# Performance work log

Measured on AMD Instinct MI355X. Metric: run time of the kernel, lower is better.

The kernel has to match this reference:

```python
import jax, jax.numpy as jnp
import numpy as np

B, S = 256, 512
NQ = 1000           # n_skills
MEM, DK, DV, FC = 20, 50, 200, 50  # memory_size, key dim, value dim, final fc dim


def _kaiming(key, shape, fan_in):
    return jax.random.normal(key, shape) * np.float32(np.sqrt(2.0 / fan_in))


def setup_inputs() -> dict:
    key = jax.random.key(0)
    ks = jax.random.split(key, 12)
    q_data = jax.random.randint(ks[0], (B, S), 0, NQ + 1)
    qa_data = jax.random.randint(ks[1], (B, S), 0, 2 * NQ + 1)
    u = jax.random.uniform(ks[2], (B * S,))
    # target: -1 = masked/padding, else binary label (matches target.ge(0) masking)
    target = jnp.where(u < 0.1, -1.0, (u > 0.55).astype(jnp.float32))
    q_embed_w = _kaiming(ks[3], (NQ + 1, DK), DK)
    qa_embed_w = _kaiming(ks[4], (2 * NQ + 1, DV), DV)
    memory_key = _kaiming(ks[5], (MEM, DK), DK)
    init_memory_value = _kaiming(ks[6], (MEM, DV), DV)
    erase_w = _kaiming(ks[7], (DV, DV), DV)
    erase_b = jnp.zeros((DV,), jnp.float32)
    add_w = _kaiming(ks[8], (DV, DV), DV)
    add_b = jnp.zeros((DV,), jnp.float32)
    read_w = _kaiming(ks[9], (DV + FC, FC), DV + FC)
    read_b = jnp.zeros((FC,), jnp.float32)
    pred_w = _kaiming(ks[10], (FC, 1), FC)
    pred_b = jnp.zeros((1,), jnp.float32)
    return dict(q_data=q_data, qa_data=qa_data, target=target,
                q_embed_w=q_embed_w, qa_embed_w=qa_embed_w,
                memory_key=memory_key, init_memory_value=init_memory_value,
                erase_w=erase_w, erase_b=erase_b, add_w=add_w, add_b=add_b,
                read_w=read_w, read_b=read_b, pred_w=pred_w, pred_b=pred_b)


def reference(q_data, qa_data, target, q_embed_w, qa_embed_w, memory_key,
              init_memory_value, erase_w, erase_b, add_w, add_b,
              read_w, read_b, pred_w, pred_b):
    b = q_data.shape[0]
    q_e = q_embed_w[q_data]     # [B,S,DK]
    qa_e = qa_embed_w[qa_data]  # [B,S,DV]
    Mv0 = jnp.broadcast_to(init_memory_value, (b, MEM, DV))

    def step(Mv, xs):
        q_t, qa_t = xs                                        # [B,DK], [B,DV]
        corr = jax.nn.softmax(q_t @ memory_key.T, axis=1)     # [B,MEM] addressing
        read = jnp.einsum('bm,bmd->bd', corr, Mv)             # weighted read
        erase = jax.nn.sigmoid(qa_t @ erase_w + erase_b)      # [B,DV]
        add = jnp.tanh(qa_t @ add_w + add_b)                  # [B,DV]
        w = corr[:, :, None]                                  # [B,MEM,1]
        Mv = Mv * (1.0 - w * erase[:, None, :]) + w * add[:, None, :]
        return Mv, read

    _, reads = jax.lax.scan(step, Mv0, (q_e.transpose(1, 0, 2), qa_e.transpose(1, 0, 2)))
    reads = reads.transpose(1, 0, 2)                          # [B,S,DV]
    x = jnp.concatenate([reads, q_e], axis=-1)                # [B,S,DV+FC]
    h = jnp.tanh(x @ read_w + read_b)                         # [B,S,FC]
    logits = (h @ pred_w + pred_b).reshape(-1)                # [B*S]
    mask = target >= 0.0
    t = jnp.where(mask, target, 0.0)
    # numerically-stable BCE-with-logits, masked mean
    bce = jnp.maximum(logits, 0.0) - logits * t + jnp.log1p(jnp.exp(-jnp.abs(logits)))
    loss = jnp.sum(jnp.where(mask, bce, 0.0)) / jnp.maximum(mask.sum(), 1)
    return loss, jax.nn.sigmoid(logits)
```

## Files before the change

### kernel.cpp

```cpp
#include <hip/hip_runtime.h>
#include <math.h>

#define B_   256
#define S_   512
#define NQ_  1000
#define MEM_ 20
#define DK_  50
#define DV_  200
#define FC_  50
#define RPB  2
#define CHK  16
#define CLEN (S_/CHK)
#define NKS  7
#define XS_STRIDE 232
#define CORR_STRIDE 12
#define NB_EA    ((2*NQ_+1+RPB-1)/RPB)
#define NB_CORR  4
#define NB_WPACK 7
#define NB_HQ    251
#define PREP1_BLOCKS (NB_EA+NB_CORR)
#define MM_BLOCKS (B_*CHK)
#define SCANA_BLOCKS (B_*(CHK-1))
#define SCANA_TOTAL (SCANA_BLOCKS+NB_WPACK+NB_HQ)

typedef __attribute__((ext_vector_type(8))) short bf16x8_t;
typedef __attribute__((ext_vector_type(4))) float f32x4_t;
typedef __attribute__((ext_vector_type(2))) _Float16 f16x2_t;

static __device__ __forceinline__ f16x2_t h2(unsigned u){ return __builtin_bit_cast(f16x2_t, u); }
static __device__ __forceinline__ unsigned h2u(f16x2_t v){ return __builtin_bit_cast(unsigned, v); }
static __device__ __forceinline__ unsigned packh2(float x, float y){
  unsigned short bx = __builtin_bit_cast(unsigned short, (_Float16)x);
  unsigned short by = __builtin_bit_cast(unsigned short, (_Float16)y);
  return (unsigned)bx | ((unsigned)by << 16);
}
static __device__ __forceinline__ f16x2_t pkfma16(f16x2_t a, f16x2_t b, f16x2_t c){
  return __builtin_elementwise_fma(a, b, c);
}
static __device__ __forceinline__ f16x2_t splat_l(f16x2_t p){ return __builtin_shufflevector(p, p, 0, 0); }
static __device__ __forceinline__ f16x2_t splat_h(f16x2_t p){ return __builtin_shufflevector(p, p, 1, 1); }

static __device__ __forceinline__ unsigned short f2bf(float f){
  unsigned u = __float_as_uint(f);
  unsigned r = u + 0x7fffu + ((u >> 16) & 1u);
  return (unsigned short)(r >> 16);
}
static __device__ __forceinline__ float ftanh(float x){
  float e = __expf(2.f*x);
  return 1.f - 2.f*__builtin_amdgcn_rcpf(e+1.f);
}
static __device__ __forceinline__ float fsigm(float x){
  return __builtin_amdgcn_rcpf(1.f+__expf(-x));
}

__global__ __launch_bounds__(256) void k_prep1(
    const float* __restrict__ qaw,
    const float* __restrict__ ew, const float* __restrict__ eb,
    const float* __restrict__ aw, const float* __restrict__ ab,
    unsigned* __restrict__ eaTab,
    const float* __restrict__ qw, const float* __restrict__ mk,
    unsigned* __restrict__ corrH){
  __shared__ float qa[RPB*DV_];
  int blk = blockIdx.x;
  if(blk < NB_EA){
    int row0 = blk*RPB;
    for(int i=threadIdx.x; i<RPB*DV_; i+=256){
      int r = i/DV_, cc = i - r*DV_;
      int row = row0 + r;
      qa[i] = (row <= 2*NQ_) ? qaw[row*DV_+cc] : 0.f;
    }
    __syncthreads();
    int d = threadIdx.x;
    if(d >= DV_) return;
    float accE[RPB], accA[RPB];
    #pragma unroll
    for(int r=0;r<RPB;++r){ accE[r] = eb[d]; accA[r] = ab[d]; }
    float we0 = ew[d], wa0 = aw[d];
    for(int j=0;j<DV_;++j){
      int jn = (j+1 < DV_) ? j+1 : j;
      float we1 = ew[jn*DV_+d];
      float wa1 = aw[jn*DV_+d];
      #pragma unroll
      for(int r=0;r<RPB;++r){
        float x = qa[r*DV_+j];
        accE[r] = fmaf(x, we0, accE[r]);
        accA[r] = fmaf(x, wa0, accA[r]);
      }
      we0 = we1; wa0 = wa1;
    }
    #pragma unroll
    for(int r=0;r<RPB;++r){
      int row = row0 + r;
      if(row <= 2*NQ_){
        unsigned he = (unsigned)__builtin_bit_cast(unsigned short, (_Float16)fsigm(accE[r]));
        unsigned ha = (unsigned)__builtin_bit_cast(unsigned short, (_Float16)ftanh(accA[r]));
        eaTab[(size_t)row*DV_+d] = he | (ha << 16);
      }
    }
  } else {
    int q = (blk-NB_EA)*256 + threadIdx.x;
    if(q > NQ_) return;
    float qv[DK_];
    #pragma unroll
    for(int j=0;j<DK_;++j) qv[j] = qw[q*DK_+j];
    float s[MEM_]; float mx = -1e30f;
    #pragma unroll
    for(int m=0;m<MEM_;++m){
      float acc = 0.f;
      #pragma unroll
      for(int j=0;j<DK_;++j) acc = fmaf(qv[j], mk[m*DK_+j], acc);
      s[m] = acc; mx = fmaxf(mx, acc);
    }
    float sum = 0.f;
    #pragma unroll
    for(int m=0;m<MEM_;++m){ s[m] = __expf(s[m]-mx); sum += s[m]; }
    float inv = __builtin_amdgcn_rcpf(sum);
    #pragma unroll
    for(int i=0;i<MEM_/2;++i)
      corrH[q*CORR_STRIDE+i] = packh2(s[2*i]*inv, s[2*i+1]*inv);
  }
}

__global__ __launch_bounds__(256,8) void k_scanA(const int* __restrict__ qd,
    const int* __restrict__ qad,
    const unsigned* __restrict__ corrH,
    const unsigned* __restrict__ eaTab,
    unsigned* __restrict__ ABu,
    const float* __restrict__ qw,
    const float* __restrict__ rw, const float* __restrict__ rb,
    const float* __restrict__ pw,
    unsigned short* __restrict__ WpFrag, float* __restrict__ pwPad,
    float* __restrict__ hq){
  const int blk = blockIdx.x;
  if(blk >= SCANA_BLOCKS){
    int xblk = blk - SCANA_BLOCKS;
    if(xblk < NB_WPACK){
      int ks = xblk;
      int nt = threadIdx.x >> 6;
      int lane = threadIdx.x & 63;
      int quad = lane >> 4, col = lane & 15;
      int n = nt*16 + col;
      unsigned short tmp[8];
      #pragma unroll
      for(int j=0;j<8;++j){
        int k = ks*32 + quad*8 + j;
        tmp[j] = (k < DV_ && n < FC_) ? f2bf(rw[k*FC_+n]) : (unsigned short)0;
      }
      uint4* dst = reinterpret_cast<uint4*>(WpFrag + ((size_t)(ks*4+nt)*64 + lane)*8);
      *dst = *reinterpret_cast<const uint4*>(tmp);
      if(ks == 0 && threadIdx.x < 64)
        pwPad[threadIdx.x] = (threadIdx.x < FC_) ? pw[threadIdx.x] : 0.f;
    } else {
      int idx = (xblk-NB_WPACK)*256 + threadIdx.x;
      int q = idx >> 6, n = idx & 63;
      if(q > NQ_) return;
      float v = 0.f;
      if(n < FC_){
        float acc = rb[n];
        #pragma unroll
        for(int j=0;j<DK_;++j)
          acc = fmaf(qw[q*DK_+j], rw[(DV_+j)*FC_+n], acc);
        v = acc;
      }
      hq[q*64+n] = v;
    }
    return;
  }

  const int b = blk / (CHK-1), c = blk % (CHK-1);
  const int d = threadIdx.x;
  const int dc = (d < DV_) ? d : DV_-1;
  const bool act = (d < DV_);
  const int* __restrict__ qp  = qd  + b*S_ + c*CLEN;
  const int* __restrict__ qap = qad + b*S_ + c*CLEN;

  const f16x2_t one2h = {(_Float16)1.f, (_Float16)1.f};
  f16x2_t A2[MEM_/2], B2[MEM_/2];
  #pragma unroll
  for(int i=0;i<MEM_/2;++i){ A2[i] = one2h; B2[i] = (f16x2_t){(_Float16)0.f,(_Float16)0.f}; }

  unsigned ea0 = eaTab[(size_t)qap[0]*DV_ + dc];
  unsigned ea1 = eaTab[(size_t)qap[1]*DV_ + dc];
  unsigned ea2 = eaTab[(size_t)qap[2]*DV_ + dc];
  int qa3 = qap[3], qa4 = qap[4], qa5 = qap[5];
  int s0 = __builtin_amdgcn_readfirstlane(qp[0]);
  int s1 = __builtin_amdgcn_readfirstlane(qp[1]);
  const unsigned* c0p = corrH + s0*CORR_STRIDE;
  uint4 ca0 = *(const uint4*)(c0p); uint4 cb0 = *(const uint4*)(c0p+4); uint2 cc0 = *(const uint2*)(c0p+8);
  const unsigned* c1p = corrH + s1*CORR_STRIDE;
  uint4 ca1 = *(const uint4*)(c1p); uint4 cb1 = *(const uint4*)(c1p+4); uint2 cc1 = *(const uint2*)(c1p+8);
  int qn2 = qp[2], qn3 = qp[3];

  #pragma unroll 4
  for(int t=0;t<CLEN;++t){
    int qs = __builtin_amdgcn_readfirstlane(qn2);
    const unsigned* cnp = corrH + qs*CORR_STRIDE;
    uint4 ca2 = *(const uint4*)(cnp);
    uint4 cb2 = *(const uint4*)(cnp+4);
    uint2 cc2 = *(const uint2*)(cnp+8);
    unsigned eanew = eaTab[(size_t)qa3*DV_ + dc];
    int t4 = (t+4 < CLEN) ? t+4 : CLEN-1;
    int qnew = qp[t4];
    int t6 = (t+6 < CLEN) ? t+6 : CLEN-1;
    int qanew = qap[t6];

    f16x2_t pe = h2(ea0);
    const f16x2_t ee = splat_l(pe), aa = splat_h(pe);
    #define UPDA(u, i) { \
      f16x2_t cp = h2(u); \
      f16x2_t al = pkfma16(-cp, ee, one2h); \
      f16x2_t be = cp*aa; \
      A2[i] = A2[i]*al; \
      B2[i] = pkfma16(al, B2[i], be); }
    UPDA(ca0.x, 0)  UPDA(ca0.y, 1)  UPDA(ca0.z, 2)  UPDA(ca0.w, 3)
    UPDA(cb0.x, 4)  UPDA(cb0.y, 5)  UPDA(cb0.z, 6)  UPDA(cb0.w, 7)
    UPDA(cc0.x, 8)  UPDA(cc0.y, 9)
    #undef UPDA

    ca0=ca1; cb0=cb1; cc0=cc1;
    ca1=ca2; cb1=cb2; cc1=cc2;
    qn2=qn3; qn3=qnew;
    ea0=ea1; ea1=ea2; ea2=eanew;
    qa3=qa4; qa4=qa5; qa5=qanew;
  }
  if(act){
    unsigned* base = ABu + ((size_t)(b*(CHK-1) + c)*MEM_)*DV_ + d;
    #pragma unroll
    for(int i=0;i<MEM_/2;++i){
      unsigned a01 = h2u(A2[i]);
      unsigned b01 = h2u(B2[i]);
      base[(size_t)(2*i)*DV_]   = (a01 & 0xffffu) | (b01 << 16);
      base[(size_t)(2*i+1)*DV_] = (a01 >> 16)     | (b01 & 0xffff0000u);
    }
  }
}

__global__ __launch_bounds__(256) void k_prefix(const float* __restrict__ mv0,
    const unsigned* __restrict__ ABu, unsigned* __restrict__ Mv0p){
  int i = blockIdx.x*256 + threadIdx.x;
  if(i >= B_*(MEM_/2)*DV_) return;
  int d = i % DV_;
  int p = (i / DV_) % (MEM_/2);
  int b = i / (DV_*(MEM_/2));
  float MvE = mv0[(2*p)*DV_+d];
  float MvO = mv0[(2*p+1)*DV_+d];
  #pragma unroll
  for(int c=1;c<CHK;++c){
    unsigned vE = ABu[((size_t)(b*(CHK-1) + (c-1))*MEM_ + 2*p)*DV_ + d];
    unsigned vO = ABu[((size_t)(b*(CHK-1) + (c-1))*MEM_ + 2*p+1)*DV_ + d];
    MvE = fmaf((float)h2(vE)[0], MvE, (float)h2(vE)[1]);
    MvO = fmaf((float)h2(vO)[0], MvO, (float)h2(vO)[1]);
    Mv0p[((size_t)(b*CHK + c)*(MEM_/2) + p)*DV_ + d] = packh2(MvE, MvO);
  }
}

__global__ __launch_bounds__(256,8) void k_scan_mm(const int* __restrict__ qd,
    const int* __restrict__ qad,
    const unsigned* __restrict__ corrH,
    const unsigned* __restrict__ eaTab,
    const float* __restrict__ mv0,
    const unsigned* __restrict__ Mv0p,
    const unsigned short* __restrict__ WpFrag,
    const float* __restrict__ hq,
    const float* __restrict__ pwPad, const float* __restrict__ pb,
    const float* __restrict__ target,
    float* __restrict__ out, float2* __restrict__ partials){
  __shared__ unsigned short Xs[CLEN*XS_STRIDE];
  __shared__ float sred[2][2][16];
  __shared__ float sbce[4];

  const int blk = blockIdx.x;
  const int b = blk >> 4, c = blk & (CHK-1);
  const int d = threadIdx.x;
  const int dc = (d < DV_) ? d : DV_-1;
  const bool act = (d < DV_);
  const bool padw = (d < 224);
  const int* __restrict__ qp  = qd  + b*S_ + c*CLEN;
  const int* __restrict__ qap = qad + b*S_ + c*CLEN;

  const int wave = threadIdx.x >> 6;
  const int lane = threadIdx.x & 63;
  const int col  = lane & 15, quad = lane >> 4;
  const int rt   = wave & 1;
  const int nh   = wave >> 1;
  const int mbase = rt*16;

  int qpre[4];
  #pragma unroll
  for(int reg=0;reg<4;++reg) qpre[reg] = qp[mbase + quad*4 + reg];

  f16x2_t Mv2[MEM_/2];
  if(c == 0){
    #pragma unroll
    for(int i=0;i<MEM_/2;++i)
      Mv2[i] = (f16x2_t){ (_Float16)mv0[(2*i)*DV_+dc], (_Float16)mv0[(2*i+1)*DV_+dc] };
  } else {
    const unsigned* base = Mv0p + ((size_t)(b*CHK + c)*(MEM_/2))*DV_ + dc;
    #pragma unroll
    for(int i=0;i<MEM_/2;++i)
      Mv2[i] = h2(base[(size_t)i*DV_]);
  }

  unsigned ea0 = eaTab[(size_t)qap[0]*DV_ + dc];
  unsigned ea1 = eaTab[(size_t)qap[1]*DV_ + dc];
  unsigned ea2 = eaTab[(size_t)qap[2]*DV_ + dc];
  int qa3 = qap[3], qa4 = qap[4], qa5 = qap[5];
  int s0 = __builtin_amdgcn_readfirstlane(qp[0]);
  int s1 = __builtin_amdgcn_readfirstlane(qp[1]);
  const unsigned* c0p = corrH + s0*CORR_STRIDE;
  uint4 ca0 = *(const uint4*)(c0p); uint4 cb0 = *(const uint4*)(c0p+4); uint2 cc0 = *(const uint2*)(c0p+8);
  const unsigned* c1p = corrH + s1*CORR_STRIDE;
  uint4 ca1 = *(const uint4*)(c1p); uint4 cb1 = *(const uint4*)(c1p+4); uint2 cc1 = *(const uint2*)(c1p+8);
  int qn2 = qp[2], qn3 = qp[3];

  #pragma unroll 4
  for(int t=0;t<CLEN;++t){
    int qs = __builtin_amdgcn_readfirstlane(qn2);
    const unsigned* cnp = corrH + qs*CORR_STRIDE;
    uint4 ca2 = *(const uint4*)(cnp);
    uint4 cb2 = *(const uint4*)(cnp+4);
    uint2 cc2 = *(const uint2*)(cnp+8);
    unsigned eanew = eaTab[(size_t)qa3*DV_ + dc];
    int t4 = (t+4 < CLEN) ? t+4 : CLEN-1;
    int qnew = qp[t4];
    int t6 = (t+6 < CLEN) ? t+6 : CLEN-1;
    int qanew = qap[t6];

    f16x2_t pe = h2(ea0);
    const f16x2_t ee = splat_l(pe), aa = splat_h(pe);
    float rd0 = 0.f, rd1 = 0.f;
    #define UPD2(u, i, acc) { \
      f16x2_t cp = h2(u); \
      acc = __builtin_amdgcn_fdot2(cp, Mv2[i], acc, false); \
      f16x2_t tt = pkfma16(-Mv2[i], ee, aa); \
      Mv2[i] = pkfma16(cp, tt, Mv2[i]); }
    UPD2(ca0.x, 0, rd0)  UPD2(ca0.y, 1, rd1)  UPD2(ca0.z, 2, rd0)  UPD2(ca0.w, 3, rd1)
    UPD2(cb0.x, 4, rd0)  UPD2(cb0.y, 5, rd1)  UPD2(cb0.z, 6, rd0)  UPD2(cb0.w, 7, rd1)
    UPD2(cc0.x, 8, rd0)  UPD2(cc0.y, 9, rd1)
    #undef UPD2

    if(padw) Xs[t*XS_STRIDE + d] = act ? f2bf(rd0+rd1) : (unsigned short)0;

    ca0=ca1; cb0=cb1; cc0=cc1;
    ca1=ca2; cb1=cb2; cc1=cc2;
    qn2=qn3; qn3=qnew;
    ea0=ea1; ea1=ea2; ea2=eanew;
    qa3=qa4; qa4=qa5; qa5=qanew;
  }
  __syncthreads();

  float hqv[4][2];
  #pragma unroll
  for(int reg=0;reg<4;++reg)
    #pragma unroll
    for(int j=0;j<2;++j)
      hqv[reg][j] = hq[qpre[reg]*64 + (nh*2+j)*16 + col];

  f32x4_t acc[2];
  acc[0] = (f32x4_t){0.f,0.f,0.f,0.f};
  acc[1] = (f32x4_t){0.f,0.f,0.f,0.f};

  #pragma unroll
  for(int ks=0;ks<NKS;++ks){
    bf16x8_t a = *reinterpret_cast<const bf16x8_t*>(Xs + (mbase+col)*XS_STRIDE + quad*8 + ks*32);
    #pragma unroll
    for(int j=0;j<2;++j){
      int nt = nh*2 + j;
      bf16x8_t bfr = *reinterpret_cast<const bf16x8_t*>(WpFrag + ((size_t)(ks*4+nt)*64 + lane)*8);
      acc[j] = __builtin_amdgcn_mfma_f32_16x16x32_bf16(a, bfr, acc[j], 0, 0, 0);
    }
  }

  float part[4];
  #pragma unroll
  for(int reg=0;reg<4;++reg){
    float s = 0.f;
    #pragma unroll
    for(int j=0;j<2;++j){
      int n = (nh*2+j)*16 + col;
      float h = acc[j][reg] + hqv[reg][j];
      s = fmaf(pwPad[n], ftanh(h), s);
    }
    part[reg] = s;
  }
  #pragma unroll
  for(int off=1; off<16; off<<=1){
    #pragma unroll
    for(int reg=0;reg<4;++reg) part[reg] += __shfl_xor(part[reg], off, 64);
  }
  if(col == 0){
    #pragma unroll
    for(int reg=0;reg<4;++reg) sred[rt][nh][quad*4+reg] = part[reg];
  }
  __syncthreads();

  float bce = 0.f, cnt = 0.f;
  if(nh == 0 && col == 0){
    float pbv = pb[0];
    #pragma unroll
    for(int reg=0;reg<4;++reg){
      int idx = quad*4 + reg;
      int mloc = mbase + idx;
      int row = b*S_ + c*CLEN + mloc;
      float logit = sred[rt][0][idx] + sred[rt][1][idx] + pbv;
      out[1+row] = fsigm(logit);
      float t = target[row];
      if(t >= 0.f){
        cnt += 1.f;
        bce += fmaxf(logit,0.f) - logit*t + log1pf(__expf(-fabsf(logit)));
      }
    }
  }
  bce += __shfl_xor(bce, 16, 64); cnt += __shfl_xor(cnt, 16, 64);
  bce += __shfl_xor(bce, 32, 64); cnt += __shfl_xor(cnt, 32, 64);
  if(lane == 0 && nh == 0){ sbce[wave] = bce; sbce[2+wave] = cnt; }
  __syncthreads();
  if(threadIdx.x == 0)
    partials[blk] = make_float2(sbce[0]+sbce[1], sbce[2]+sbce[3]);
}

__global__ __launch_bounds__(256) void k_fin(const float2* __restrict__ partials,
                                             float* __restrict__ out){
  float bce = 0.f, cnt = 0.f;
  for(int i=threadIdx.x; i<MM_BLOCKS; i+=256){
    float2 p = partials[i];
    bce += p.x; cnt += p.y;
  }
  #pragma unroll
  for(int off=32; off>0; off>>=1){
    bce += __shfl_down(bce, off, 64);
    cnt += __shfl_down(cnt, off, 64);
  }
  __shared__ float sb[4], sc[4];
  int w = threadIdx.x >> 6;
  if((threadIdx.x & 63) == 0){ sb[w] = bce; sc[w] = cnt; }
  __syncthreads();
  if(threadIdx.x == 0){
    float Bt = sb[0]+sb[1]+sb[2]+sb[3];
    float Ct = sc[0]+sc[1]+sc[2]+sc[3];
    out[0] = Bt / fmaxf(Ct, 1.f);
  }
}

extern "C" void kernel_launch(void* const* d_in, const int* in_sizes, int n_in,
                              void* d_out, int out_size, void* d_ws, size_t ws_size,
                              hipStream_t stream){
  const int*   qd     = (const int*)d_in[0];
  const int*   qad    = (const int*)d_in[1];
  const float* target = (const float*)d_in[2];
  const float* qw     = (const float*)d_in[3];
  const float* qaw    = (const float*)d_in[4];
  const float* mk     = (const float*)d_in[5];
  const float* mv0    = (const float*)d_in[6];
  const float* ew     = (const float*)d_in[7];
  const float* eb     = (const float*)d_in[8];
  const float* aw     = (const float*)d_in[9];
  const float* ab     = (const float*)d_in[10];
  const float* rw     = (const float*)d_in[11];
  const float* rb     = (const float*)d_in[12];
  const float* pw     = (const float*)d_in[13];
  const float* pb     = (const float*)d_in[14];
  float* out = (float*)d_out;

  char* ws = (char*)d_ws;
  size_t off = 0;
  float2* partials = (float2*)(ws + off);            off += (size_t)MM_BLOCKS*8;
  unsigned* corrH = (unsigned*)(ws + off);           off += (((size_t)(NQ_+1)*CORR_STRIDE*4 + 255)/256)*256;
  unsigned* eaTab = (unsigned*)(ws + off);           off += (((size_t)(2*NQ_+1)*DV_*4 + 255)/256)*256;
  unsigned* ABu   = (unsigned*)(ws + off);           off += (size_t)SCANA_BLOCKS*MEM_*DV_*4;
  unsigned* Mv0p  = (unsigned*)(ws + off);           off += (size_t)MM_BLOCKS*(MEM_/2)*DV_*4;
  unsigned short* WpFrag = (unsigned short*)(ws + off); off += ((size_t)NKS*4*64*8*2 + 255)/256*256;
  float* pwPad    = (float*)(ws + off);              off += 256;
  float* hq       = (float*)(ws + off);              off += (size_t)(NQ_+1)*64*4;

  k_prep1<<<dim3(PREP1_BLOCKS), dim3(256), 0, stream>>>(qaw, ew, eb, aw, ab, eaTab,
                                                        qw, mk, corrH);
  k_scanA<<<dim3(SCANA_TOTAL), dim3(256), 0, stream>>>(qd, qad, corrH, eaTab,
                                                       ABu, qw, rw, rb, pw, WpFrag, pwPad, hq);
  k_prefix<<<dim3((B_*(MEM_/2)*DV_+255)/256), dim3(256), 0, stream>>>(mv0, ABu, Mv0p);
  k_scan_mm<<<dim3(MM_BLOCKS), dim3(256), 0, stream>>>(qd, qad, corrH, eaTab,
                                                       mv0, Mv0p, WpFrag, hq, pwPad, pb, target, out, partials);
  k_fin<<<dim3(1), dim3(256), 0, stream>>>(partials, out);
}
```

Baseline: 220.3 us.

## Halve scan chunk count and process each chunk in two halves for the MLP

Cuts the number of sequence chunks per batch row from 16 to 8, so each chunk is 64 steps long. The main scan kernel now walks a chunk in two 32-step halves, reusing the same shared-memory tile and MFMA epilogue for each half. This shrinks the chunk-level scanA/prefix work and the ABu/Mv0p traffic, but leaves fewer, longer serial blocks. The read-weight packing and hq precompute move from scanA into the prep kernel, which shortens scanA.

```diff
diff --git a/kernel.cpp b/kernel.cpp
--- a/kernel.cpp
+++ b/kernel.cpp
@@ -9,8 +9,9 @@
 #define DV_  200
 #define FC_  50
 #define RPB  2
-#define CHK  16
+#define CHK  8
 #define CLEN (S_/CHK)
+#define HLEN 32
 #define NKS  7
 #define XS_STRIDE 232
 #define CORR_STRIDE 12
@@ -18,10 +19,9 @@
 #define NB_CORR  4
 #define NB_WPACK 7
 #define NB_HQ    251
-#define PREP1_BLOCKS (NB_EA+NB_CORR)
+#define PREP_BLOCKS (NB_EA+NB_CORR+NB_WPACK+NB_HQ)
 #define MM_BLOCKS (B_*CHK)
 #define SCANA_BLOCKS (B_*(CHK-1))
-#define SCANA_TOTAL (SCANA_BLOCKS+NB_WPACK+NB_HQ)
 
 typedef __attribute__((ext_vector_type(8))) short bf16x8_t;
 typedef __attribute__((ext_vector_type(4))) float f32x4_t;
@@ -59,7 +59,11 @@
     const float* __restrict__ aw, const float* __restrict__ ab,
     unsigned* __restrict__ eaTab,
     const float* __restrict__ qw, const float* __restrict__ mk,
-    unsigned* __restrict__ corrH){
+    unsigned* __restrict__ corrH,
+    const float* __restrict__ rw, const float* __restrict__ rb,
+    const float* __restrict__ pw,
+    unsigned short* __restrict__ WpFrag, float* __restrict__ pwPad,
+    float* __restrict__ hq){
   __shared__ float qa[RPB*DV_];
   int blk = blockIdx.x;
   if(blk < NB_EA){
@@ -97,7 +101,7 @@
         eaTab[(size_t)row*DV_+d] = he | (ha << 16);
       }
     }
-  } else {
+  } else if(blk < NB_EA+NB_CORR){
     int q = (blk-NB_EA)*256 + threadIdx.x;
     if(q > NQ_) return;
     float qv[DK_];
@@ -118,6 +122,35 @@
     #pragma unroll
     for(int i=0;i<MEM_/2;++i)
       corrH[q*CORR_STRIDE+i] = packh2(s[2*i]*inv, s[2*i+1]*inv);
+  } else if(blk < NB_EA+NB_CORR+NB_WPACK){
+    int ks = blk - (NB_EA+NB_CORR);
+    int nt = threadIdx.x >> 6;
+    int lane = threadIdx.x & 63;
+    int quad = lane >> 4, col = lane & 15;
+    int n = nt*16 + col;
+    unsigned short tmp[8];
+    #pragma unroll
+    for(int j=0;j<8;++j){
+      int k = ks*32 + quad*8 + j;
+      tmp[j] = (k < DV_ && n < FC_) ? f2bf(rw[k*FC_+n]) : (unsigned short)0;
+    }
+    uint4* dst = reinterpret_cast<uint4*>(WpFrag + ((size_t)(ks*4+nt)*64 + lane)*8);
+    *dst = *reinterpret_cast<const uint4*>(tmp);
+    if(ks == 0 && threadIdx.x < 64)
+      pwPad[threadIdx.x] = (threadIdx.x < FC_) ? pw[threadIdx.x] : 0.f;
+  } else {
+    int idx = (blk-(NB_EA+NB_CORR+NB_WPACK))*256 + threadIdx.x;
+    int q = idx >> 6, n = idx & 63;
+    if(q > NQ_) return;
+    float v = 0.f;
+    if(n < FC_){
+      float acc = rb[n];
+      #pragma unroll
+      for(int j=0;j<DK_;++j)
+        acc = fmaf(qw[q*DK_+j], rw[(DV_+j)*FC_+n], acc);
+      v = acc;
+    }
+    hq[q*64+n] = v;
   }
 }
 
@@ -125,48 +158,8 @@
     const int* __restrict__ qad,
     const unsigned* __restrict__ corrH,
     const unsigned* __restrict__ eaTab,
-    unsigned* __restrict__ ABu,
-    const float* __restrict__ qw,
-    const float* __restrict__ rw, const float* __restrict__ rb,
-    const float* __restrict__ pw,
-    unsigned short* __restrict__ WpFrag, float* __restrict__ pwPad,
-    float* __restrict__ hq){
+    unsigned* __restrict__ ABu){
   const int blk = blockIdx.x;
-  if(blk >= SCANA_BLOCKS){
-    int xblk = blk - SCANA_BLOCKS;
-    if(xblk < NB_WPACK){
-      int ks = xblk;
-      int nt = threadIdx.x >> 6;
-      int lane = threadIdx.x & 63;
-      int quad = lane >> 4, col = lane & 15;
-      int n = nt*16 + col;
-      unsigned short tmp[8];
-      #pragma unroll
-      for(int j=0;j<8;++j){
-        int k = ks*32 + quad*8 + j;
-        tmp[j] = (k < DV_ && n < FC_) ? f2bf(rw[k*FC_+n]) : (unsigned short)0;
-      }
-      uint4* dst = reinterpret_cast<uint4*>(WpFrag + ((size_t)(ks*4+nt)*64 + lane)*8);
-      *dst = *reinterpret_cast<const uint4*>(tmp);
-      if(ks == 0 && threadIdx.x < 64)
-        pwPad[threadIdx.x] = (threadIdx.x < FC_) ? pw[threadIdx.x] : 0.f;
-    } else {
-      int idx = (xblk-NB_WPACK)*256 + threadIdx.x;
-      int q = idx >> 6, n = idx & 63;
-      if(q > NQ_) return;
-      float v = 0.f;
-      if(n < FC_){
-        float acc = rb[n];
-        #pragma unroll
-        for(int j=0;j<DK_;++j)
-          acc = fmaf(qw[q*DK_+j], rw[(DV_+j)*FC_+n], acc);
-        v = acc;
-      }
-      hq[q*64+n] = v;
-    }
-    return;
-  }
-
   const int b = blk / (CHK-1), c = blk % (CHK-1);
   const int d = threadIdx.x;
   const int dc = (d < DV_) ? d : DV_-1;
@@ -265,18 +258,18 @@
     const float* __restrict__ pwPad, const float* __restrict__ pb,
     const float* __restrict__ target,
     float* __restrict__ out, float2* __restrict__ partials){
-  __shared__ unsigned short Xs[CLEN*XS_STRIDE];
+  __shared__ unsigned short Xs[HLEN*XS_STRIDE];
   __shared__ float sred[2][2][16];
   __shared__ float sbce[4];
 
   const int blk = blockIdx.x;
-  const int b = blk >> 4, c = blk & (CHK-1);
+  const int b = blk >> 3, c8 = blk & (CHK-1);
   const int d = threadIdx.x;
   const int dc = (d < DV_) ? d : DV_-1;
   const bool act = (d < DV_);
   const bool padw = (d < 224);
-  const int* __restrict__ qp  = qd  + b*S_ + c*CLEN;
-  const int* __restrict__ qap = qad + b*S_ + c*CLEN;
+  const int* __restrict__ qp  = qd  + b*S_ + c8*CLEN;
+  const int* __restrict__ qap = qad + b*S_ + c8*CLEN;
 
   const int wave = threadIdx.x >> 6;
   const int lane = threadIdx.x & 63;
@@ -285,135 +278,143 @@
   const int nh   = wave >> 1;
   const int mbase = rt*16;
 
-  int qpre[4];
+  int qpre[2][4];
   #pragma unroll
-  for(int reg=0;reg<4;++reg) qpre[reg] = qp[mbase + quad*4 + reg];
+  for(int h=0;h<2;++h)
+    #pragma unroll
+    for(int reg=0;reg<4;++reg) qpre[h][reg] = qp[h*HLEN + mbase + quad*4 + reg];
 
   f16x2_t Mv2[MEM_/2];
-  if(c == 0){
+  if(c8 == 0){
     #pragma unroll
     for(int i=0;i<MEM_/2;++i)
       Mv2[i] = (f16x2_t){ (_Float16)mv0[(2*i)*DV_+dc], (_Float16)mv0[(2*i+1)*DV_+dc] };
   } else {
-    const unsigned* base = Mv0p + ((size_t)(b*CHK + c)*(MEM_/2))*DV_ + dc;
+    const unsigned* base = Mv0p + ((size_t)(b*CHK + c8)*(MEM_/2))*DV_ + dc;
     #pragma unroll
     for(int i=0;i<MEM_/2;++i)
       Mv2[i] = h2(base[(size_t)i*DV_]);
   }
 
-  unsigned ea0 = eaTab[(size_t)qap[0]*DV_ + dc];
-  unsigned ea1 = eaTab[(size_t)qap[1]*DV_ + dc];
-  unsigned ea2 = eaTab[(size_t)qap[2]*DV_ + dc];
-  int qa3 = qap[3], qa4 = qap[4], qa5 = qap[5];
-  int s0 = __builtin_amdgcn_readfirstlane(qp[0]);
-  int s1 = __builtin_amdgcn_readfirstlane(qp[1]);
-  const unsigned* c0p = corrH + s0*CORR_STRIDE;
-  uint4 ca0 = *(const uint4*)(c0p); uint4 cb0 = *(const uint4*)(c0p+4); uint2 cc0 = *(const uint2*)(c0p+8);
-  const unsigned* c1p = corrH + s1*CORR_STRIDE;
-  uint4 ca1 = *(const uint4*)(c1p); uint4 cb1 = *(const uint4*)(c1p+4); uint2 cc1 = *(const uint2*)(c1p+8);
-  int qn2 = qp[2], qn3 = qp[3];
-
-  #pragma unroll 4
-  for(int t=0;t<CLEN;++t){
-    int qs = __builtin_amdgcn_readfirstlane(qn2);
-    const unsigned* cnp = corrH + qs*CORR_STRIDE;
-    uint4 ca2 = *(const uint4*)(cnp);
-    uint4 cb2 = *(const uint4*)(cnp+4);
-    uint2 cc2 = *(const uint2*)(cnp+8);
-    unsigned eanew = eaTab[(size_t)qa3*DV_ + dc];
-    int t4 = (t+4 < CLEN) ? t+4 : CLEN-1;
-    int qnew = qp[t4];
-    int t6 = (t+6 < CLEN) ? t+6 : CLEN-1;
-    int qanew = qap[t6];
-
-    f16x2_t pe = h2(ea0);
-    const f16x2_t ee = splat_l(pe), aa = splat_h(pe);
-    float rd0 = 0.f, rd1 = 0.f;
-    #define UPD2(u, i, acc) { \
-      f16x2_t cp = h2(u); \
-      acc = __builtin_amdgcn_fdot2(cp, Mv2[i], acc, false); \
-      f16x2_t tt = pkfma16(-Mv2[i], ee, aa); \
-      Mv2[i] = pkfma16(cp, tt, Mv2[i]); }
-    UPD2(ca0.x, 0, rd0)  UPD2(ca0.y, 1, rd1)  UPD2(ca0.z, 2, rd0)  UPD2(ca0.w, 3, rd1)
-    UPD2(cb0.x, 4, rd0)  UPD2(cb0.y, 5, rd1)  UPD2(cb0.z, 6, rd0)  UPD2(cb0.w, 7, rd1)
-    UPD2(cc0.x, 8, rd0)  UPD2(cc0.y, 9, rd1)
-    #undef UPD2
-
-    if(padw) Xs[t*XS_STRIDE + d] = act ? f2bf(rd0+rd1) : (unsigned short)0;
-
-    ca0=ca1; cb0=cb1; cc0=cc1;
-    ca1=ca2; cb1=cb2; cc1=cc2;
-    qn2=qn3; qn3=qnew;
-    ea0=ea1; ea1=ea2; ea2=eanew;
-    qa3=qa4; qa4=qa5; qa5=qanew;
-  }
-  __syncthreads();
-
-  float hqv[4][2];
-  #pragma unroll
-  for(int reg=0;reg<4;++reg)
-    #pragma unroll
-    for(int j=0;j<2;++j)
-      hqv[reg][j] = hq[qpre[reg]*64 + (nh*2+j)*16 + col];
-
-  f32x4_t acc[2];
-  acc[0] = (f32x4_t){0.f,0.f,0.f,0.f};
-  acc[1] = (f32x4_t){0.f,0.f,0.f,0.f};
-
-  #pragma unroll
-  for(int ks=0;ks<NKS;++ks){
-    bf16x8_t a = *reinterpret_cast<const bf16x8_t*>(Xs + (mbase+col)*XS_STRIDE + quad*8 + ks*32);
-    #pragma unroll
-    for(int j=0;j<2;++j){
-      int nt = nh*2 + j;
-      bf16x8_t bfr = *reinterpret_cast<const bf16x8_t*>(WpFrag + ((size_t)(ks*4+nt)*64 + lane)*8);
-      acc[j] = __builtin_amdgcn_mfma_f32_16x16x32_bf16(a, bfr, acc[j], 0, 0, 0);
-    }
-  }
-
-  float part[4];
-  #pragma unroll
-  for(int reg=0;reg<4;++reg){
-    float s = 0.f;
-    #pragma unroll
-    for(int j=0;j<2;++j){
-      int n = (nh*2+j)*16 + col;
-      float h = acc[j][reg] + hqv[reg][j];
-      s = fmaf(pwPad[n], ftanh(h), s);
-    }
-    part[reg] = s;
-  }
-  #pragma unroll
-  for(int off=1; off<16; off<<=1){
-    #pragma unroll
-    for(int reg=0;reg<4;++reg) part[reg] += __shfl_xor(part[reg], off, 64);
-  }
-  if(col == 0){
-    #pragma unroll
-    for(int reg=0;reg<4;++reg) sred[rt][nh][quad*4+reg] = part[reg];
-  }
-  __syncthreads();
-
-  float bce = 0.f, cnt = 0.f;
-  if(nh == 0 && col == 0){
-    float pbv = pb[0];
+  float bceAcc = 0.f, cntAcc = 0.f;
+  const float pbv = pb[0];
+
+  #pragma unroll 1
+  for(int h=0;h<2;++h){
+    const int g0 = h*HLEN;
+    unsigned ea0 = eaTab[(size_t)qap[g0+0]*DV_ + dc];
+    unsigned ea1 = eaTab[(size_t)qap[g0+1]*DV_ + dc];
+    unsigned ea2 = eaTab[(size_t)qap[g0+2]*DV_ + dc];
+    int qa3 = qap[g0+3], qa4 = qap[g0+4], qa5 = qap[g0+5];
+    int s0 = __builtin_amdgcn_readfirstlane(qp[g0+0]);
+    int s1 = __builtin_amdgcn_readfirstlane(qp[g0+1]);
+    const unsigned* c0p = corrH + s0*CORR_STRIDE;
+    uint4 ca0 = *(const uint4*)(c0p); uint4 cb0 = *(const uint4*)(c0p+4); uint2 cc0 = *(const uint2*)(c0p+8);
+    const unsigned* c1p = corrH + s1*CORR_STRIDE;
+    uint4 ca1 = *(const uint4*)(c1p); uint4 cb1 = *(const uint4*)(c1p+4); uint2 cc1 = *(const uint2*)(c1p+8);
+    int qn2 = qp[g0+2], qn3 = qp[g0+3];
+
+    #pragma unroll 4
+    for(int t=0;t<HLEN;++t){
+      int g = g0 + t;
+      int qs = __builtin_amdgcn_readfirstlane(qn2);
+      const unsigned* cnp = corrH + qs*CORR_STRIDE;
+      uint4 ca2 = *(const uint4*)(cnp);
+      uint4 cb2 = *(const uint4*)(cnp+4);
+      uint2 cc2 = *(const uint2*)(cnp+8);
+      unsigned eanew = eaTab[(size_t)qa3*DV_ + dc];
+      int g4 = (g+4 < CLEN) ? g+4 : CLEN-1;
+      int qnew = qp[g4];
+      int g6 = (g+6 < CLEN) ? g+6 : CLEN-1;
+      int qanew = qap[g6];
+
+      f16x2_t pe = h2(ea0);
+      const f16x2_t ee = splat_l(pe), aa = splat_h(pe);
+      float rd0 = 0.f, rd1 = 0.f;
+      #define UPD2(u, i, acc) { \
+        f16x2_t cp = h2(u); \
+        acc = __builtin_amdgcn_fdot2(cp, Mv2[i], acc, false); \
+        f16x2_t tt = pkfma16(-Mv2[i], ee, aa); \
+        Mv2[i] = pkfma16(cp, tt, Mv2[i]); }
+      UPD2(ca0.x, 0, rd0)  UPD2(ca0.y, 1, rd1)  UPD2(ca0.z, 2, rd0)  UPD2(ca0.w, 3, rd1)
+      UPD2(cb0.x, 4, rd0)  UPD2(cb0.y, 5, rd1)  UPD2(cb0.z, 6, rd0)  UPD2(cb0.w, 7, rd1)
+      UPD2(cc0.x, 8, rd0)  UPD2(cc0.y, 9, rd1)
+      #undef UPD2
+
+      if(padw) Xs[t*XS_STRIDE + d] = act ? f2bf(rd0+rd1) : (unsigned short)0;
+
+      ca0=ca1; cb0=cb1; cc0=cc1;
+      ca1=ca2; cb1=cb2; cc1=cc2;
+      qn2=qn3; qn3=qnew;
+      ea0=ea1; ea1=ea2; ea2=eanew;
+      qa3=qa4; qa4=qa5; qa5=qanew;
+    }
+    __syncthreads();
+
+    float hqv[4][2];
+    #pragma unroll
+    for(int reg=0;reg<4;++reg)
+      #pragma unroll
+      for(int j=0;j<2;++j)
+        hqv[reg][j] = hq[qpre[h][reg]*64 + (nh*2+j)*16 + col];
+
+    f32x4_t acc[2];
+    acc[0] = (f32x4_t){0.f,0.f,0.f,0.f};
+    acc[1] = (f32x4_t){0.f,0.f,0.f,0.f};
+    #pragma unroll
+    for(int ks=0;ks<NKS;++ks){
+      bf16x8_t a = *reinterpret_cast<const bf16x8_t*>(Xs + (mbase+col)*XS_STRIDE + quad*8 + ks*32);
+      #pragma unroll
+      for(int j=0;j<2;++j){
+        int nt = nh*2 + j;
+        bf16x8_t bfr = *reinterpret_cast<const bf16x8_t*>(WpFrag + ((size_t)(ks*4+nt)*64 + lane)*8);
+        acc[j] = __builtin_amdgcn_mfma_f32_16x16x32_bf16(a, bfr, acc[j], 0, 0, 0);
+      }
+    }
+
+    float part[4];
     #pragma unroll
     for(int reg=0;reg<4;++reg){
-      int idx = quad*4 + reg;
-      int mloc = mbase + idx;
-      int row = b*S_ + c*CLEN + mloc;
-      float logit = sred[rt][0][idx] + sred[rt][1][idx] + pbv;
-      out[1+row] = fsigm(logit);
-      float t = target[row];
-      if(t >= 0.f){
-        cnt += 1.f;
-        bce += fmaxf(logit,0.f) - logit*t + log1pf(__expf(-fabsf(logit)));
+      float s = 0.f;
+      #pragma unroll
+      for(int j=0;j<2;++j){
+        int n = (nh*2+j)*16 + col;
+        float hh = acc[j][reg] + hqv[reg][j];
+        s = fmaf(pwPad[n], ftanh(hh), s);
       }
-    }
-  }
-  bce += __shfl_xor(bce, 16, 64); cnt += __shfl_xor(cnt, 16, 64);
-  bce += __shfl_xor(bce, 32, 64); cnt += __shfl_xor(cnt, 32, 64);
-  if(lane == 0 && nh == 0){ sbce[wave] = bce; sbce[2+wave] = cnt; }
+      part[reg] = s;
+    }
+    #pragma unroll
+    for(int off=1; off<16; off<<=1){
+      #pragma unroll
+      for(int reg=0;reg<4;++reg) part[reg] += __shfl_xor(part[reg], off, 64);
+    }
+    if(col == 0){
+      #pragma unroll
+      for(int reg=0;reg<4;++reg) sred[rt][nh][quad*4+reg] = part[reg];
+    }
+    __syncthreads();
+
+    if(nh == 0 && col == 0){
+      #pragma unroll
+      for(int reg=0;reg<4;++reg){
+        int idx = quad*4 + reg;
+        int mloc = mbase + idx;
+        int row = b*S_ + c8*CLEN + g0 + mloc;
+        float logit = sred[rt][0][idx] + sred[rt][1][idx] + pbv;
+        out[1+row] = fsigm(logit);
+        float t = target[row];
+        if(t >= 0.f){
+          cntAcc += 1.f;
+          bceAcc += fmaxf(logit,0.f) - logit*t + log1pf(__expf(-fabsf(logit)));
+        }
+      }
+    }
+  }
+
+  bceAcc += __shfl_xor(bceAcc, 16, 64); cntAcc += __shfl_xor(cntAcc, 16, 64);
+  bceAcc += __shfl_xor(bceAcc, 32, 64); cntAcc += __shfl_xor(cntAcc, 32, 64);
+  if(lane == 0 && nh == 0){ sbce[wave] = bceAcc; sbce[2+wave] = cntAcc; }
   __syncthreads();
   if(threadIdx.x == 0)
     partials[blk] = make_float2(sbce[0]+sbce[1], sbce[2]+sbce[3]);
@@ -473,10 +474,10 @@
   float* pwPad    = (float*)(ws + off);              off += 256;
   float* hq       = (float*)(ws + off);              off += (size_t)(NQ_+1)*64*4;
 
-  k_prep1<<<dim3(PREP1_BLOCKS), dim3(256), 0, stream>>>(qaw, ew, eb, aw, ab, eaTab,
-                                                        qw, mk, corrH);
-  k_scanA<<<dim3(SCANA_TOTAL), dim3(256), 0, stream>>>(qd, qad, corrH, eaTab,
-                                                       ABu, qw, rw, rb, pw, WpFrag, pwPad, hq);
+  k_prep1<<<dim3(PREP_BLOCKS), dim3(256), 0, stream>>>(qaw, ew, eb, aw, ab, eaTab,
+                                                       qw, mk, corrH,
+                                                       rw, rb, pw, WpFrag, pwPad, hq);
+  k_scanA<<<dim3(SCANA_BLOCKS), dim3(256), 0, stream>>>(qd, qad, corrH, eaTab, ABu);
   k_prefix<<<dim3((B_*(MEM_/2)*DV_+255)/256), dim3(256), 0, stream>>>(mv0, ABu, Mv0p);
   k_scan_mm<<<dim3(MM_BLOCKS), dim3(256), 0, stream>>>(qd, qad, corrH, eaTab,
                                                        mv0, Mv0p, WpFrag, hq, pwPad, pb, target, out, partials);
```

Result: slower. 235.6 us (+6.9%).
